# Performance work log

Measured on AMD Instinct MI355X. Metric: run time of the kernel, lower is better.

## Reference

```python
import jax, jax.numpy as jnp
import numpy as np

N_NODES = 50000
N_EDGES = 600000
F_IN = 128   # nfeature
H = 128      # nhidden (must equal nfeature due to original code's gcn2 init)
C = 10       # nclass


def setup_inputs() -> dict:
    key = jax.random.key(0)
    ks = jax.random.split(key, 8)
    row = jax.random.randint(ks[0], (N_EDGES,), 0, N_NODES)
    col = jax.random.randint(ks[1], (N_EDGES,), 0, N_NODES)
    label = jax.random.randint(ks[2], (N_EDGES,), 0, C)
    features = jax.random.normal(ks[3], (N_NODES, F_IN), dtype=jnp.float32)
    s1 = 1.0 / np.sqrt(F_IN)
    W1 = jax.random.uniform(ks[4], (H, F_IN), jnp.float32, -s1, s1)
    b1 = jnp.zeros((H,), jnp.float32)
    s2 = 1.0 / np.sqrt(H)
    W2 = jax.random.uniform(ks[5], (H, H), jnp.float32, -s2, s2)
    b2 = jnp.zeros((H,), jnp.float32)
    s3 = 1.0 / np.sqrt(2 * H)
    Wfc = jax.random.uniform(ks[6], (C, 2 * H), jnp.float32, -s3, s3)
    bfc = jnp.zeros((C,), jnp.float32)
    return {"features": features, "W1": W1, "b1": b1, "W2": W2, "b2": b2,
            "Wfc": Wfc, "bfc": bfc, "row": row, "col": col, "label": label}


def gcn_conv(x, row, col, W, b):
    # GCNConv: add self loops, linear, then deg-normalized scatter-add.
    n = x.shape[0]
    sl = jnp.arange(n, dtype=row.dtype)
    r = jnp.concatenate([row, sl])  # source / j index (PyG edge_index[0])
    c = jnp.concatenate([col, sl])  # target / aggregation index (edge_index[1])
    h = x @ W.T + b  # [N, H]
    # degree computed over row of self-loop-augmented edge_index (>=1 always)
    deg = jax.ops.segment_sum(jnp.ones(r.shape, h.dtype), r, num_segments=n)
    dinv = deg ** -0.5
    norm = dinv[r] * dinv[c]  # [E+N]
    msg = norm[:, None] * h[r]  # gather + scale, [E+N, H]
    return jax.ops.segment_sum(msg, c, num_segments=n)  # scatter-add, [N, H]


def reference(features, W1, b1, W2, b2, Wfc, bfc, row, col, label):
    h1 = gcn_conv(features, row, col, W1, b1)  # [N, H]
    h2 = gcn_conv(h1, row, col, W2, b2)        # [N, H]
    # take_logits: index_select per edge endpoint, concat on feature dim
    x = jnp.concatenate([h2[row], h2[col]], axis=1)  # [E, 2H]
    logits = x @ Wfc.T + bfc  # [E, C]
    logp = jax.nn.log_softmax(logits, axis=-1)
    loss = -jnp.mean(jnp.take_along_axis(logp, label[:, None], axis=1))
    return loss, logits
```

## Files before the change

### kernel.cpp

```cpp
#include <hip/hip_runtime.h>
#include <hip/hip_bf16.h>
#include <math.h>

#define NND 50000
#define NE  600000
#define HD  128
#define NC  10
#define CAP 64
#define NCH 64
#define ECHUNK 9375
#define HBIN8 25000
#define SCB 128
#define HISTB 256
#define COLB 32
#define GEMMB 782
#define PFXB 49
#define LOSSB 2344
#define TSTRIDE 32
#define PSTRIDE 16

typedef unsigned short ushort_t;
typedef unsigned char uchar_t;
typedef __attribute__((ext_vector_type(8))) short short8;
typedef __attribute__((ext_vector_type(4))) float f32x4;

__device__ __forceinline__ float bf2f(unsigned short u) {
  return __uint_as_float(((unsigned int)u) << 16);
}
__device__ __forceinline__ unsigned short f2bf(float f) {
  __hip_bfloat16 h = __float2bfloat16(f);
  return *(unsigned short*)&h;
}

__device__ __forceinline__ short8 f2bf8(const float* __restrict__ p) {
  float4 x0 = *(const float4*)p;
  float4 x1 = *(const float4*)(p + 4);
  short8 v;
  v[0] = (short)f2bf(x0.x); v[1] = (short)f2bf(x0.y);
  v[2] = (short)f2bf(x0.z); v[3] = (short)f2bf(x0.w);
  v[4] = (short)f2bf(x1.x); v[5] = (short)f2bf(x1.y);
  v[6] = (short)f2bf(x1.z); v[7] = (short)f2bf(x1.w);
  return v;
}

__global__ __launch_bounds__(256) void k_prep(const int* __restrict__ row,
                                              const int* __restrict__ col,
                                              uchar_t* __restrict__ partC,
                                              uchar_t* __restrict__ partR,
                                              uchar_t* __restrict__ loc8,
                                              const float* __restrict__ W1,
                                              const float* __restrict__ W2,
                                              const float* __restrict__ Wfc,
                                              const float* __restrict__ b1,
                                              const float* __restrict__ b2,
                                              float* __restrict__ M,
                                              float* __restrict__ uv) {
  int bb = blockIdx.x, tid = threadIdx.x;
  if (bb < HISTB) {
    __shared__ unsigned int h32[HBIN8 / 4];
    bool isCol = (bb < SCB);
    const int* src = isCol ? col : row;
    uchar_t* dst = isCol ? partC : partR;
    int hb = bb & (SCB - 1);
    int cb = hb & 63, half = hb >> 6;
    int binbase = half * HBIN8;
    for (int i = tid; i < HBIN8 / 4; i += 256) h32[i] = 0;
    __syncthreads();
    int e0 = cb * ECHUNK;
    if (isCol) {
      for (int e = e0 + tid; e < e0 + ECHUNK; e += 256) {
        int r = src[e] - binbase;
        if (r >= 0 && r < HBIN8) {
          unsigned int old = atomicAdd(&h32[r >> 2], 1u << ((r & 3) * 8));
          loc8[e] = (uchar_t)((old >> ((r & 3) * 8)) & 0xff);
        }
      }
    } else {
      for (int e = e0 + tid; e < e0 + ECHUNK; e += 256) {
        int r = src[e] - binbase;
        if (r >= 0 && r < HBIN8)
          atomicAdd(&h32[r >> 2], 1u << ((r & 3) * 8));
      }
    }
    __syncthreads();
    unsigned int* d32 = (unsigned int*)(dst + (size_t)hb * HBIN8);
    for (int i = tid; i < HBIN8 / 4; i += 256) d32[i] = h32[i];
  } else {
    __shared__ float V[128];
    int c5 = bb - HISTB;
    int grp = c5 >> 4, n = c5 & 15;
    bool valid = (n < NC);
    const float* wrow = &Wfc[(valid ? n : 0) * 256 + grp * 128];
    if (tid < 128) {
      float s = 0.f;
      for (int m = 0; m < 128; m++) s += wrow[m] * W2[m * HD + tid];
      V[tid] = s;
    }
    __syncthreads();
    if (tid < 128) {
      float t = 0.f;
      for (int k = 0; k < 128; k++) t += V[k] * W1[k * HD + tid];
      M[(grp * 16 + n) * HD + tid] = valid ? t : 0.f;
    } else if (tid == 128 && valid) {
      float t = 0.f;
      for (int k = 0; k < 128; k++) t += V[k] * b1[k];
      uv[grp * 10 + n] = t;
    } else if (tid == 129 && valid) {
      float t = 0.f;
      for (int k = 0; k < 128; k++) t += wrow[k] * b2[k];
      uv[20 + grp * 10 + n] = t;
    }
  }
}

__global__ __launch_bounds__(256) void k_mid(const uchar_t* __restrict__ partC,
                                             const uchar_t* __restrict__ partR,
                                             uchar_t* __restrict__ off8,
                                             int* __restrict__ pos,
                                             float* __restrict__ dinv,
                                             const float* __restrict__ features,
                                             const float* __restrict__ M,
                                             ushort_t* __restrict__ T0,
                                             float* __restrict__ out) {
  int bb = blockIdx.x, tid = threadIdx.x;
  if (bb < GEMMB) {
    int bid = bb;
    int w = tid >> 6, lane = tid & 63;
    int m = lane & 15, q = lane >> 4;
    short8 B[8];
    #pragma unroll
    for (int g = 0; g < 8; g++) {
      int grp = g >> 2, t = g & 3;
      B[g] = f2bf8(&M[(grp * 16 + m) * HD + t * 32 + q * 8]);
    }
    int rowbase = bid * 64 + w * 16;
    int rm = rowbase + m; if (rm >= NND) rm = NND - 1;
    short8 a[4];
    #pragma unroll
    for (int t = 0; t < 4; t++)
      a[t] = f2bf8(&features[(long)rm * HD + t * 32 + q * 8]);
    f32x4 accL = {0.f, 0.f, 0.f, 0.f}, accR = {0.f, 0.f, 0.f, 0.f};
    #pragma unroll
    for (int t = 0; t < 4; t++) {
      accL = __builtin_amdgcn_mfma_f32_16x16x32_bf16(a[t], B[t],     accL, 0, 0, 0);
      accR = __builtin_amdgcn_mfma_f32_16x16x32_bf16(a[t], B[4 + t], accR, 0, 0, 0);
    }
    #pragma unroll
    for (int reg = 0; reg < 4; reg++) {
      int r = rowbase + q * 4 + reg;
      if (r < NND) {
        float vL = (m < 10) ? accL[reg] : ((m == 10) ? 1.0f : 0.0f);
        float vR = (m < 10) ? accR[reg] : 0.0f;
        T0[(long)r * TSTRIDE + m]      = f2bf(vL);
        T0[(long)r * TSTRIDE + 16 + m] = f2bf(vR);
      }
    }
  } else {
    int idx = (bb - GEMMB) * 256 + tid;
    if (idx == 0) out[0] = 0.f;
    if (idx < NND / 4) {
      int n4 = idx * 4;
      int half = (n4 >= HBIN8) ? 1 : 0;
      int local = n4 - half * HBIN8;
      unsigned int runs = 0;
      #pragma unroll 8
      for (int cb = 0; cb < NCH; cb++) {
        unsigned int cv = *(const unsigned int*)&partC[(size_t)(half * NCH + cb) * HBIN8 + local];
        *(unsigned int*)&off8[(size_t)cb * NND + n4] = runs;
        runs += cv;
      }
      int4 pv;
      pv.x = runs & 0xff; pv.y = (runs >> 8) & 0xff;
      pv.z = (runs >> 16) & 0xff; pv.w = runs >> 24;
      *(int4*)&pos[n4] = pv;
      unsigned int rs = 0;
      #pragma unroll 8
      for (int cb = 0; cb < NCH; cb++)
        rs += *(const unsigned int*)&partR[(size_t)(half * NCH + cb) * HBIN8 + local];
      float4 dv;
      dv.x = rsqrtf(1.0f + (float)(rs & 0xff));
      dv.y = rsqrtf(1.0f + (float)((rs >> 8) & 0xff));
      dv.z = rsqrtf(1.0f + (float)((rs >> 16) & 0xff));
      dv.w = rsqrtf(1.0f + (float)(rs >> 24));
      *(float4*)&dinv[n4] = dv;
    }
  }
}

__global__ __launch_bounds__(256) void k_scat(const int* __restrict__ row,
                                              const int* __restrict__ col,
                                              const uchar_t* __restrict__ loc8,
                                              const uchar_t* __restrict__ off8,
                                              ushort_t* __restrict__ srcs) {
  int e = blockIdx.x * 256 + threadIdx.x;
  if (e < NE) {
    int c = col[e];
    int cb = e / ECHUNK;
    int p = (int)off8[(size_t)cb * NND + c] + (int)loc8[e];
    if (p < CAP) srcs[(size_t)c * CAP + p] = (ushort_t)row[e];
  }
}

template <bool FINAL>
__global__ __launch_bounds__(256) void k_aggrn(const ushort_t* __restrict__ Q,
                                               const ushort_t* __restrict__ srcs,
                                               const int* __restrict__ pos,
                                               const float* __restrict__ dinv,
                                               ushort_t* __restrict__ T1,
                                               float* __restrict__ Pr,
                                               float* __restrict__ Pc,
                                               const float* __restrict__ uv) {
  int g = threadIdx.x >> 5, lane = threadIdx.x & 31;
  int half = lane >> 4;
  int f = lane & 15;
  int node = blockIdx.x * 8 + g;
  if (node >= NND) return;
  float di = dinv[node];
  unsigned int qv = *(const unsigned int*)&Q[(long)node * TSTRIDE + 2 * f];
  float sw = (half == 0) ? di * di : 0.f;
  float a0 = sw * bf2f((ushort_t)(qv & 0xffff));
  float a1 = sw * bf2f((ushort_t)(qv >> 16));
  int cnt = pos[node]; if (cnt > CAP) cnt = CAP;
  const ushort_t* nb = &srcs[(long)node * CAP];
  for (int base = 0; base < cnt; base += 32) {
    int m2 = cnt - base; if (m2 > 32) m2 = 32;
    int sl = 0; float wl = 0.f;
    if (lane < m2) { sl = (int)nb[base + lane]; wl = di * dinv[sl]; }
    int iters = (m2 + 1) >> 1;
    int u = 0;
    for (; u + 1 < iters; u += 2) {
      int t0 = 2 * u + half, t1 = t0 + 2;
      int s0 = __shfl(sl, t0 & 31, 32); float w0 = __shfl(wl, t0 & 31, 32);
      int s1 = __shfl(sl, t1 & 31, 32); float w1 = __shfl(wl, t1 & 31, 32);
      unsigned int h0 = *(const unsigned int*)&Q[(long)s0 * TSTRIDE + 2 * f];
      unsigned int h1 = *(const unsigned int*)&Q[(long)s1 * TSTRIDE + 2 * f];
      a0 += w0 * bf2f((ushort_t)(h0 & 0xffff));
      a1 += w0 * bf2f((ushort_t)(h0 >> 16));
      a0 += w1 * bf2f((ushort_t)(h1 & 0xffff));
      a1 += w1 * bf2f((ushort_t)(h1 >> 16));
    }
    if (u < iters) {
      int t = 2 * u + half;
      int s = __shfl(sl, t & 31, 32); float wv = __shfl(wl, t & 31, 32);
      unsigned int hs = *(const unsigned int*)&Q[(long)s * TSTRIDE + 2 * f];
      a0 += wv * bf2f((ushort_t)(hs & 0xffff));
      a1 += wv * bf2f((ushort_t)(hs >> 16));
    }
  }
  a0 += __shfl(a0, f + 16, 32);
  a1 += __shfl(a1, f + 16, 32);
  if (FINAL) {
    float s_i = __shfl(bf2f((ushort_t)(qv & 0xffff)), 5, 32);
    float z2  = __shfl(a0, 5, 32);
    if (half == 0) {
      if (f < 5) {
        int cc = 2 * f;
        float2 v;
        v.x = a0 + z2 * uv[cc]     + s_i * uv[20 + cc];
        v.y = a1 + z2 * uv[cc + 1] + s_i * uv[20 + cc + 1];
        *(float2*)&Pr[(long)node * PSTRIDE + cc] = v;
      } else if (f >= 8 && f < 13) {
        int cc = 2 * f - 16;
        float2 v;
        v.x = a0 + z2 * uv[10 + cc]     + s_i * uv[30 + cc];
        v.y = a1 + z2 * uv[10 + cc + 1] + s_i * uv[30 + cc + 1];
        *(float2*)&Pc[(long)node * PSTRIDE + cc] = v;
      }
    }
  } else {
    if (half == 0) {
      unsigned int o = ((unsigned int)f2bf(a1) << 16) | (unsigned int)f2bf(a0);
      *(unsigned int*)&T1[(long)node * TSTRIDE + 2 * f] = o;
    }
  }
}

__global__ __launch_bounds__(256) void k_edge(const float* __restrict__ Pr,
                                              const float* __restrict__ Pc,
                                              const int* __restrict__ row,
                                              const int* __restrict__ col,
                                              const int* __restrict__ label,
                                              const float* __restrict__ bfc,
                                              float* __restrict__ logits,
                                              float* __restrict__ out) {
  __shared__ __align__(16) float S[2560];
  __shared__ float Ls[4];
  int tid = threadIdx.x;
  long e0 = (long)blockIdx.x * 256;
  int e = (int)e0 + tid;
  float lp = 0.f;
  if (e < NE) {
    int r = row[e], c = col[e];
    const float* pr = &Pr[(long)r * PSTRIDE];
    const float* pc = &Pc[(long)c * PSTRIDE];
    float4 r0 = *(const float4*)&pr[0];
    float4 r1 = *(const float4*)&pr[4];
    float4 r2 = *(const float4*)&pr[8];
    float4 c0 = *(const float4*)&pc[0];
    float4 c1 = *(const float4*)&pc[4];
    float4 c2 = *(const float4*)&pc[8];
    float p[NC];
    p[0] = r0.x + c0.x + bfc[0]; p[1] = r0.y + c0.y + bfc[1];
    p[2] = r0.z + c0.z + bfc[2]; p[3] = r0.w + c0.w + bfc[3];
    p[4] = r1.x + c1.x + bfc[4]; p[5] = r1.y + c1.y + bfc[5];
    p[6] = r1.z + c1.z + bfc[6]; p[7] = r1.w + c1.w + bfc[7];
    p[8] = r2.x + c2.x + bfc[8]; p[9] = r2.y + c2.y + bfc[9];
    #pragma unroll
    for (int cc = 0; cc < NC; cc++) S[tid * 10 + cc] = p[cc];
    float mx = p[0];
    #pragma unroll
    for (int cc = 1; cc < NC; cc++) mx = fmaxf(mx, p[cc]);
    float se = 0.f;
    #pragma unroll
    for (int cc = 0; cc < NC; cc++) se += __expf(p[cc] - mx);
    int lb = label[e];
    float plb = p[0];
    #pragma unroll
    for (int cc = 1; cc < NC; cc++) plb = (cc == lb) ? p[cc] : plb;
    lp = plb - mx - __logf(se);
  }
  __syncthreads();
  int ve = NE - (int)e0; if (ve > 256) ve = 256;
  int limF4 = ve * 10 / 4;
  float4* dst = (float4*)&logits[e0 * 10];
  const float4* src4 = (const float4*)S;
  for (int i = tid; i < limF4; i += 256) dst[i] = src4[i];
  #pragma unroll
  for (int off = 32; off > 0; off >>= 1) lp += __shfl_xor(lp, off, 64);
  if ((tid & 63) == 0) Ls[tid >> 6] = lp;
  __syncthreads();
  if (tid == 0)
    atomicAdd(out, -(Ls[0] + Ls[1] + Ls[2] + Ls[3]) / (float)NE);
}

extern "C" void kernel_launch(void* const* d_in, const int* in_sizes, int n_in,
                              void* d_out, int out_size, void* d_ws, size_t ws_size,
                              hipStream_t stream) {
  const float* features = (const float*)d_in[0];
  const float* W1  = (const float*)d_in[1];
  const float* b1  = (const float*)d_in[2];
  const float* W2  = (const float*)d_in[3];
  const float* b2  = (const float*)d_in[4];
  const float* Wfc = (const float*)d_in[5];
  const float* bfc = (const float*)d_in[6];
  const int* row   = (const int*)d_in[7];
  const int* col   = (const int*)d_in[8];
  const int* label = (const int*)d_in[9];
  float* out = (float*)d_out;

  float* ws = (float*)d_ws;
  size_t o = 0;
  int* pos = (int*)(ws + o);            o += 50048;
  float* dinv = ws + o;                 o += 50048;
  ushort_t* srcs = (ushort_t*)(ws + o); o += (size_t)NND * CAP / 2;
  uchar_t* partC = (uchar_t*)(ws + o);  o += SCB * HBIN8 / 4;
  uchar_t* partR = (uchar_t*)(ws + o);  o += SCB * HBIN8 / 4;
  uchar_t* off8  = (uchar_t*)(ws + o);  o += NCH * NND / 4;
  uchar_t* loc8  = (uchar_t*)(ws + o);  o += NE / 4;
  float* Pr = ws + o;                   o += (size_t)NND * PSTRIDE;
  float* Pc = ws + o;                   o += (size_t)NND * PSTRIDE;
  float* uv = ws + o;                   o += 64;
  float* M  = ws + o;                   o += 4096;
  ushort_t* T0 = (ushort_t*)(ws + o);   o += (size_t)NND * TSTRIDE / 2;
  ushort_t* T1 = (ushort_t*)(ws + o);   o += (size_t)NND * TSTRIDE / 2;

  k_prep<<<HISTB + COLB, 256, 0, stream>>>(row, col, partC, partR, loc8,
                                           W1, W2, Wfc, b1, b2, M, uv);
  k_mid<<<GEMMB + PFXB, 256, 0, stream>>>(partC, partR, off8, pos, dinv,
                                          features, M, T0, out);
  k_scat<<<LOSSB, 256, 0, stream>>>(row, col, loc8, off8, srcs);
  k_aggrn<false><<<6250, 256, 0, stream>>>(T0, srcs, pos, dinv, T1, nullptr, nullptr, uv);
  k_aggrn<true><<<6250, 256, 0, stream>>>(T1, srcs, pos, dinv, nullptr, Pr, Pc, uv);
  k_edge<<<LOSSB, 256, 0, stream>>>(Pr, Pc, row, col, label, bfc, out + 1, out);
}
```

Measured before the change: 203.0 us.

## Widen neighbor gathers to 16-byte loads and precompute per-edge source weights

The aggregation kernel now has each 32-lane group handle eight neighbors at once, with each of four sub-lanes loading a uint4 (8 bf16 values) per neighbor row instead of 32-bit loads. Partial sums are reduced across row groups with xor shuffles. The scatter kernel also stores dinv of each source next to its index, so the aggregation loads it contiguously instead of doing a dependent random gather. This cuts load instruction count and removes a gather, at the cost of an extra NND*CAP float array that must be written and read, plus more shuffles in the reduction.

```diff
diff --git a/kernel.cpp b/kernel.cpp
--- a/kernel.cpp
+++ b/kernel.cpp
@@ -191,86 +191,119 @@
                                               const int* __restrict__ col,
                                               const uchar_t* __restrict__ loc8,
                                               const uchar_t* __restrict__ off8,
-                                              ushort_t* __restrict__ srcs) {
+                                              const float* __restrict__ dinv,
+                                              ushort_t* __restrict__ srcs,
+                                              float* __restrict__ wsrc) {
   int e = blockIdx.x * 256 + threadIdx.x;
   if (e < NE) {
-    int c = col[e];
+    int c = col[e], r = row[e];
     int cb = e / ECHUNK;
     int p = (int)off8[(size_t)cb * NND + c] + (int)loc8[e];
-    if (p < CAP) srcs[(size_t)c * CAP + p] = (ushort_t)row[e];
+    if (p < CAP) {
+      srcs[(size_t)c * CAP + p] = (ushort_t)r;
+      wsrc[(size_t)c * CAP + p] = dinv[r];
+    }
   }
 }
 
 template <bool FINAL>
 __global__ __launch_bounds__(256) void k_aggrn(const ushort_t* __restrict__ Q,
                                                const ushort_t* __restrict__ srcs,
+                                               const float* __restrict__ wsrc,
                                                const int* __restrict__ pos,
                                                const float* __restrict__ dinv,
                                                ushort_t* __restrict__ T1,
                                                float* __restrict__ Pr,
                                                float* __restrict__ Pc,
                                                const float* __restrict__ uv) {
-  int g = threadIdx.x >> 5, lane = threadIdx.x & 31;
-  int half = lane >> 4;
-  int f = lane & 15;
-  int node = blockIdx.x * 8 + g;
+  int lane = threadIdx.x & 31;
+  int rg = lane >> 2, sub = lane & 3;
+  int node = blockIdx.x * 8 + (threadIdx.x >> 5);
   if (node >= NND) return;
   float di = dinv[node];
-  unsigned int qv = *(const unsigned int*)&Q[(long)node * TSTRIDE + 2 * f];
-  float sw = (half == 0) ? di * di : 0.f;
-  float a0 = sw * bf2f((ushort_t)(qv & 0xffff));
-  float a1 = sw * bf2f((ushort_t)(qv >> 16));
+  uint4 qv4 = *(const uint4*)&Q[(long)node * TSTRIDE + sub * 8];
+  float own[8];
+  own[0] = bf2f((ushort_t)(qv4.x & 0xffff)); own[1] = bf2f((ushort_t)(qv4.x >> 16));
+  own[2] = bf2f((ushort_t)(qv4.y & 0xffff)); own[3] = bf2f((ushort_t)(qv4.y >> 16));
+  own[4] = bf2f((ushort_t)(qv4.z & 0xffff)); own[5] = bf2f((ushort_t)(qv4.z >> 16));
+  own[6] = bf2f((ushort_t)(qv4.w & 0xffff)); own[7] = bf2f((ushort_t)(qv4.w >> 16));
+  float sw = (rg == 0) ? di * di : 0.f;
+  float acc[8];
+  #pragma unroll
+  for (int j = 0; j < 8; j++) acc[j] = sw * own[j];
   int cnt = pos[node]; if (cnt > CAP) cnt = CAP;
   const ushort_t* nb = &srcs[(long)node * CAP];
+  const float* ws = &wsrc[(long)node * CAP];
   for (int base = 0; base < cnt; base += 32) {
     int m2 = cnt - base; if (m2 > 32) m2 = 32;
     int sl = 0; float wl = 0.f;
-    if (lane < m2) { sl = (int)nb[base + lane]; wl = di * dinv[sl]; }
-    int iters = (m2 + 1) >> 1;
-    int u = 0;
-    for (; u + 1 < iters; u += 2) {
-      int t0 = 2 * u + half, t1 = t0 + 2;
-      int s0 = __shfl(sl, t0 & 31, 32); float w0 = __shfl(wl, t0 & 31, 32);
-      int s1 = __shfl(sl, t1 & 31, 32); float w1 = __shfl(wl, t1 & 31, 32);
-      unsigned int h0 = *(const unsigned int*)&Q[(long)s0 * TSTRIDE + 2 * f];
-      unsigned int h1 = *(const unsigned int*)&Q[(long)s1 * TSTRIDE + 2 * f];
-      a0 += w0 * bf2f((ushort_t)(h0 & 0xffff));
-      a1 += w0 * bf2f((ushort_t)(h0 >> 16));
-      a0 += w1 * bf2f((ushort_t)(h1 & 0xffff));
-      a1 += w1 * bf2f((ushort_t)(h1 >> 16));
-    }
-    if (u < iters) {
-      int t = 2 * u + half;
-      int s = __shfl(sl, t & 31, 32); float wv = __shfl(wl, t & 31, 32);
-      unsigned int hs = *(const unsigned int*)&Q[(long)s * TSTRIDE + 2 * f];
-      a0 += wv * bf2f((ushort_t)(hs & 0xffff));
-      a1 += wv * bf2f((ushort_t)(hs >> 16));
-    }
-  }
-  a0 += __shfl(a0, f + 16, 32);
-  a1 += __shfl(a1, f + 16, 32);
+    if (lane < m2) { sl = (int)nb[base + lane]; wl = di * ws[base + lane]; }
+    for (int u = 0; u * 8 < m2; u++) {
+      int ridx = u * 8 + rg;
+      int s = __shfl(sl, ridx, 32);
+      float w = __shfl(wl, ridx, 32);
+      if (ridx < m2) {
+        uint4 h = *(const uint4*)&Q[(long)s * TSTRIDE + sub * 8];
+        acc[0] += w * bf2f((ushort_t)(h.x & 0xffff)); acc[1] += w * bf2f((ushort_t)(h.x >> 16));
+        acc[2] += w * bf2f((ushort_t)(h.y & 0xffff)); acc[3] += w * bf2f((ushort_t)(h.y >> 16));
+        acc[4] += w * bf2f((ushort_t)(h.z & 0xffff)); acc[5] += w * bf2f((ushort_t)(h.z >> 16));
+        acc[6] += w * bf2f((ushort_t)(h.w & 0xffff)); acc[7] += w * bf2f((ushort_t)(h.w >> 16));
+      }
+    }
+  }
+  #pragma unroll
+  for (int off = 4; off <= 16; off <<= 1) {
+    #pragma unroll
+    for (int j = 0; j < 8; j++) acc[j] += __shfl_xor(acc[j], off, 32);
+  }
   if (FINAL) {
-    float s_i = __shfl(bf2f((ushort_t)(qv & 0xffff)), 5, 32);
-    float z2  = __shfl(a0, 5, 32);
-    if (half == 0) {
-      if (f < 5) {
-        int cc = 2 * f;
+    float s_i = __shfl(own[2], 1, 32);
+    float z2  = __shfl(acc[2], 1, 32);
+    if (rg == 0) {
+      if (sub == 0) {
+        float4 v0, v1;
+        v0.x = acc[0] + z2 * uv[0] + s_i * uv[20];
+        v0.y = acc[1] + z2 * uv[1] + s_i * uv[21];
+        v0.z = acc[2] + z2 * uv[2] + s_i * uv[22];
+        v0.w = acc[3] + z2 * uv[3] + s_i * uv[23];
+        v1.x = acc[4] + z2 * uv[4] + s_i * uv[24];
+        v1.y = acc[5] + z2 * uv[5] + s_i * uv[25];
+        v1.z = acc[6] + z2 * uv[6] + s_i * uv[26];
+        v1.w = acc[7] + z2 * uv[7] + s_i * uv[27];
+        *(float4*)&Pr[(long)node * PSTRIDE]     = v0;
+        *(float4*)&Pr[(long)node * PSTRIDE + 4] = v1;
+      } else if (sub == 1) {
         float2 v;
-        v.x = a0 + z2 * uv[cc]     + s_i * uv[20 + cc];
-        v.y = a1 + z2 * uv[cc + 1] + s_i * uv[20 + cc + 1];
-        *(float2*)&Pr[(long)node * PSTRIDE + cc] = v;
-      } else if (f >= 8 && f < 13) {
-        int cc = 2 * f - 16;
+        v.x = acc[0] + z2 * uv[8] + s_i * uv[28];
+        v.y = acc[1] + z2 * uv[9] + s_i * uv[29];
+        *(float2*)&Pr[(long)node * PSTRIDE + 8] = v;
+      } else if (sub == 2) {
+        float4 v0, v1;
+        v0.x = acc[0] + z2 * uv[10] + s_i * uv[30];
+        v0.y = acc[1] + z2 * uv[11] + s_i * uv[31];
+        v0.z = acc[2] + z2 * uv[12] + s_i * uv[32];
+        v0.w = acc[3] + z2 * uv[13] + s_i * uv[33];
+        v1.x = acc[4] + z2 * uv[14] + s_i * uv[34];
+        v1.y = acc[5] + z2 * uv[15] + s_i * uv[35];
+        v1.z = acc[6] + z2 * uv[16] + s_i * uv[36];
+        v1.w = acc[7] + z2 * uv[17] + s_i * uv[37];
+        *(float4*)&Pc[(long)node * PSTRIDE]     = v0;
+        *(float4*)&Pc[(long)node * PSTRIDE + 4] = v1;
+      } else {
         float2 v;
-        v.x = a0 + z2 * uv[10 + cc]     + s_i * uv[30 + cc];
-        v.y = a1 + z2 * uv[10 + cc + 1] + s_i * uv[30 + cc + 1];
-        *(float2*)&Pc[(long)node * PSTRIDE + cc] = v;
+        v.x = acc[0] + z2 * uv[18] + s_i * uv[38];
+        v.y = acc[1] + z2 * uv[19] + s_i * uv[39];
+        *(float2*)&Pc[(long)node * PSTRIDE + 8] = v;
       }
     }
   } else {
-    if (half == 0) {
-      unsigned int o = ((unsigned int)f2bf(a1) << 16) | (unsigned int)f2bf(a0);
-      *(unsigned int*)&T1[(long)node * TSTRIDE + 2 * f] = o;
+    if (rg == 0) {
+      uint4 o;
+      o.x = (unsigned int)f2bf(acc[0]) | ((unsigned int)f2bf(acc[1]) << 16);
+      o.y = (unsigned int)f2bf(acc[2]) | ((unsigned int)f2bf(acc[3]) << 16);
+      o.z = (unsigned int)f2bf(acc[4]) | ((unsigned int)f2bf(acc[5]) << 16);
+      o.w = (unsigned int)f2bf(acc[6]) | ((unsigned int)f2bf(acc[7]) << 16);
+      *(uint4*)&T1[(long)node * TSTRIDE + sub * 8] = o;
     }
   }
 }
@@ -353,6 +386,7 @@
   int* pos = (int*)(ws + o);            o += 50048;
   float* dinv = ws + o;                 o += 50048;
   ushort_t* srcs = (ushort_t*)(ws + o); o += (size_t)NND * CAP / 2;
+  float* wsrc = ws + o;                 o += (size_t)NND * CAP;
   uchar_t* partC = (uchar_t*)(ws + o);  o += SCB * HBIN8 / 4;
   uchar_t* partR = (uchar_t*)(ws + o);  o += SCB * HBIN8 / 4;
   uchar_t* off8  = (uchar_t*)(ws + o);  o += NCH * NND / 4;
@@ -368,8 +402,8 @@
                                            W1, W2, Wfc, b1, b2, M, uv);
   k_mid<<<GEMMB + PFXB, 256, 0, stream>>>(partC, partR, off8, pos, dinv,
                                           features, M, T0, out);
-  k_scat<<<LOSSB, 256, 0, stream>>>(row, col, loc8, off8, srcs);
-  k_aggrn<false><<<6250, 256, 0, stream>>>(T0, srcs, pos, dinv, T1, nullptr, nullptr, uv);
-  k_aggrn<true><<<6250, 256, 0, stream>>>(T1, srcs, pos, dinv, nullptr, Pr, Pc, uv);
+  k_scat<<<LOSSB, 256, 0, stream>>>(row, col, loc8, off8, dinv, srcs, wsrc);
+  k_aggrn<false><<<6250, 256, 0, stream>>>(T0, srcs, wsrc, pos, dinv, T1, nullptr, nullptr, uv);
+  k_aggrn<true><<<6250, 256, 0, stream>>>(T1, srcs, wsrc, pos, dinv, nullptr, Pr, Pc, uv);
   k_edge<<<LOSSB, 256, 0, stream>>>(Pr, Pc, row, col, label, bfc, out + 1, out);
 }
```

Measured after the change: 202.6 us. No clear change (-0.2%).
